# Performance work log

Measured on AMD Instinct MI355X. Metric: run time of the kernel, lower is better.

## Reference

```python
import jax, jax.numpy as jnp
import numpy as np

F_IN, F_OUT, H, L_ENC, L_DEC, HORIZON = 32, 8, 64, 2, 2, 48
B, T = 2048, 512


def _lstm_cell(x, h, c, Wih, Whh, bih, bhh):
    # PyTorch LSTMCell: gates ordered i, f, g, o
    g = x @ Wih.T + bih + h @ Whh.T + bhh
    i, f, gg, o = jnp.split(g, 4, axis=-1)
    c_new = jax.nn.sigmoid(f) * c + jax.nn.sigmoid(i) * jnp.tanh(gg)
    h_new = jax.nn.sigmoid(o) * jnp.tanh(c_new)
    return h_new, c_new


def setup_inputs() -> dict:
    key = jax.random.key(0)
    ks = jax.random.split(key, 16)
    s = 1.0 / np.sqrt(H)
    u = lambda k, shape: jax.random.uniform(k, shape, jnp.float32, -s, s)
    return {
        "X": jax.random.normal(ks[0], (B, T, F_IN), jnp.float32),
        "X_mask": jnp.ones((B, T, F_IN), jnp.float32),
        "W_emb": u(ks[1], (H, F_IN)),
        "b_emb": u(ks[2], (H,)),
        "enc_Wih": u(ks[3], (L_ENC, 4 * H, H)),
        "enc_Whh": u(ks[4], (L_ENC, 4 * H, H)),
        "enc_bih": u(ks[5], (L_ENC, 4 * H)),
        "enc_bhh": u(ks[6], (L_ENC, 4 * H)),
        "dec_Wih": u(ks[7], (L_DEC, 4 * H, H)),
        "dec_Whh": u(ks[8], (L_DEC, 4 * H, H)),
        "dec_bih": u(ks[9], (L_DEC, 4 * H)),
        "dec_bhh": u(ks[10], (L_DEC, 4 * H)),
        "W_reg": u(ks[11], (F_OUT, H)),
        "b_reg": u(ks[12], (F_OUT,)),
    }


def reference(X, X_mask, W_emb, b_emb, enc_Wih, enc_Whh, enc_bih, enc_bhh,
              dec_Wih, dec_Whh, dec_bih, dec_bhh, W_reg, b_reg):
    batch = X.shape[0]
    # Token embedding for all timesteps at once: [T, B, H]
    emb = jnp.einsum('btf,hf->tbh', X, W_emb) + b_emb

    h0 = jnp.zeros((L_ENC, batch, H), X.dtype)
    c0 = jnp.zeros((L_ENC, batch, H), X.dtype)

    def enc_step(carry, x_t):
        h, c = carry
        h_t = x_t
        hs, cs = [], []
        for i in range(L_ENC):
            h_t, c_t = _lstm_cell(h_t, h[i], c[i], enc_Wih[i], enc_Whh[i], enc_bih[i], enc_bhh[i])
            hs.append(h_t)
            cs.append(c_t)
        return (jnp.stack(hs), jnp.stack(cs)), None

    (h_enc, _), _ = jax.lax.scan(enc_step, (h0, c0), emb)

    # Decoder: hidden states initialized from encoder h, cells from zero
    c_dec0 = jnp.zeros((L_DEC, batch, H), X.dtype)

    def dec_step(carry, _):
        h, c = carry
        h_t = h[-1]
        hs, cs = [], []
        for i in range(L_DEC):
            h_t, c_t = _lstm_cell(h_t, h[i], c[i], dec_Wih[i], dec_Whh[i], dec_bih[i], dec_bhh[i])
            hs.append(h_t)
            cs.append(c_t)
        y_t = h_t @ W_reg.T + b_reg
        return (jnp.stack(hs), jnp.stack(cs)), y_t

    _, ys = jax.lax.scan(dec_step, (h_enc, c_dec0), None, length=HORIZON)
    return jnp.transpose(ys, (1, 0, 2))  # [B, horizon, F_OUT]
```

## Files before the change

kernel.cpp:

```cpp
#include <hip/hip_runtime.h>
#include <hip/hip_bf16.h>

typedef __bf16 bf16x8 __attribute__((ext_vector_type(8)));
typedef float  f32x4  __attribute__((ext_vector_type(4)));

#define MFMA16(a,b,c) __builtin_amdgcn_mfma_f32_16x16x32_bf16((a),(b),(c),0,0,0)

#if __has_builtin(__builtin_amdgcn_exp2f)
#define EXP2(x) __builtin_amdgcn_exp2f(x)
#else
#define EXP2(x) exp2f(x)
#endif
#define RCP(x) __builtin_amdgcn_rcpf(x)

#define KL  1.44269504088896340736f
#define K2L 2.88539008177792681472f

__device__ __forceinline__ bf16x8 cvt8(f32x4 a, f32x4 b){
  bf16x8 r;
  r[0]=(__bf16)a[0]; r[1]=(__bf16)a[1]; r[2]=(__bf16)a[2]; r[3]=(__bf16)a[3];
  r[4]=(__bf16)b[0]; r[5]=(__bf16)b[1]; r[6]=(__bf16)b[2]; r[7]=(__bf16)b[3];
  return r;
}
__device__ __forceinline__ f32x4 sp(float v){ return (f32x4){v,v,v,v}; }
__device__ __forceinline__ bf16x8 ld8(const float* p){
  return cvt8(*(const f32x4*)p, *(const f32x4*)(p+4));
}
__device__ __forceinline__ bf16x8 ld8s(const float* p, float s){
  f32x4 a = *(const f32x4*)p, b = *(const f32x4*)(p+4);
  return cvt8(a*sp(s), b*sp(s));
}

__device__ __forceinline__ float lstm_ew(float gi, float gf, float gg,
                                         float go, float& c){
  float Ef = EXP2(-gf);
  float Ei = EXP2(-gi);
  float gc = fminf(fmaxf(gg, -60.f), 60.f);
  float G  = EXP2(gc);
  float Rf = RCP(1.f + Ef);
  float Rig= RCP((1.f + Ei) * (1.f + G));
  c = c*Rf + (G - 1.f)*Rig;
  float Eo = EXP2(-go);
  float ch = fminf(fmaxf(c, -30.f), 30.f);
  float C2 = EXP2(ch * K2L);
  return (C2 - 1.f) * RCP((1.f + Eo) * (1.f + C2));
}

__device__ __forceinline__ float dppx8(float v){
  return __int_as_float(__builtin_amdgcn_update_dpp(
      0, __float_as_int(v), 0x128, 0xF, 0xF, true));
}
__device__ __forceinline__ float swz4(float v){
  return __int_as_float(__builtin_amdgcn_ds_swizzle(__float_as_int(v), 0x101F));
}

extern "C" __global__ void __launch_bounds__(1024, 4)
seq2seq_kernel(const float* __restrict__ X,
               const float* __restrict__ Wemb, const float* __restrict__ bemb,
               const float* __restrict__ eWih, const float* __restrict__ eWhh,
               const float* __restrict__ ebih, const float* __restrict__ ebhh,
               const float* __restrict__ dWih, const float* __restrict__ dWhh,
               const float* __restrict__ dbih, const float* __restrict__ dbhh,
               const float* __restrict__ Wreg, const float* __restrict__ breg,
               float* __restrict__ out)
{
  __shared__ __align__(16) __bf16 XA[2][8][136];
  __shared__ __align__(16) __bf16 H1s[2][8][72];

  const int tid  = (int)threadIdx.x;
  const int w    = tid >> 6;
  const int grp  = w >> 3;
  const bool g0  = (grp == 0);
  const int wt   = w & 7;
  const int lane = tid & 63;
  const int col  = lane & 15;
  const int quad = lane >> 4;
  const int row8 = col & 7;
  const int b0   = (int)blockIdx.x * 8;
  const int brow = b0 + row8;

  const bool hib = (col & 8) != 0;
  const bool qhb = (quad & 2) != 0;
  const int  ewr = 4*(quad & 1) + (hib ? 1 : 0) + (qhb ? 2 : 0);
  const int  ewu = 8*wt + (col & 7);

  for (int i = tid; i < 2*8*136; i += 1024) (&XA[0][0][0])[i]  = (__bf16)0.f;
  for (int i = tid; i < 2*8*72;  i += 1024) (&H1s[0][0][0])[i] = (__bf16)0.f;

  bf16x8 wf[8];
  float  gb[2];
#pragma unroll
  for (int ti=0; ti<2; ++ti){
    const int gate = 2*ti + (col>>3);
    const int n = 64*gate + 8*wt + (col&7);
    const float sc = (gate == 2) ? K2L : KL;
    gb[ti] = (ebih[grp*256+n] + ebhh[grp*256+n]) * sc;
#pragma unroll
    for (int ks=0; ks<4; ++ks){
      const float* srcw = (ks < 2) ? eWih : eWhh;
      wf[ti*4+ks] = ld8s(srcw + ((size_t)(grp*256+n))*64 + (ks&1)*32 + quad*8, sc);
    }
  }

  const int ue = (w&3)*16 + col;
  bf16x8 wembf;
  float eb = 0.f;
  const float* xb = X + (size_t)brow*512*32 + quad*8;
  f32x4 pa0, pb0, pa1, pb1;
  if (w < 4){
    wembf = ld8(Wemb + ue*32 + quad*8);
    eb = bemb[ue];
    pa1 = *(const f32x4*)(xb+32); pb1 = *(const f32x4*)(xb+36);
    pa0 = *(const f32x4*)(xb+64); pb0 = *(const f32x4*)(xb+68);
  }

  float cC = 0.f;

  auto EWF = [&](f32x4 A0, f32x4 A1, float& c) -> float {
    float lo0 = qhb ? A0[2] : A0[0];
    float hi0 = qhb ? A0[3] : A0[1];
    float lo1 = qhb ? A1[2] : A1[0];
    float hi1 = qhb ? A1[3] : A1[1];
    float a0s = hib ? hi0 : lo0, a0x = hib ? lo0 : hi0;
    float a1s = hib ? hi1 : lo1, a1x = hib ? lo1 : hi1;
    float r0 = dppx8(a0x), r1 = dppx8(a1x);
    float gi = hib ? r0  : a0s;
    float gf = hib ? a0s : r0;
    float gg = hib ? r1  : a1s;
    float go = hib ? a1s : r1;
    return lstm_ew(gi, gf, gg, go, c);
  };

  auto FUSED0 = [&](const int I){
    const int Px = (I+1)&1, Pr = I&1;
    bf16x8 ax0 = *(const bf16x8*)&XA[Px][row8][ 0 + quad*8];
    bf16x8 ax1 = *(const bf16x8*)&XA[Px][row8][32 + quad*8];
    bf16x8 ah0 = *(const bf16x8*)&XA[Pr][row8][64 + quad*8];
    bf16x8 ah1 = *(const bf16x8*)&XA[Pr][row8][96 + quad*8];
    f32x4 A0 = sp(gb[0]), A1 = sp(gb[1]);
    A0=MFMA16(ax0,wf[0],A0); A1=MFMA16(ax0,wf[4],A1);
    A0=MFMA16(ax1,wf[1],A0); A1=MFMA16(ax1,wf[5],A1);
    A0=MFMA16(ah0,wf[2],A0); A1=MFMA16(ah0,wf[6],A1);
    A0=MFMA16(ah1,wf[3],A0); A1=MFMA16(ah1,wf[7],A1);
    if (I < 510 && w < 4){
      const int s = I&1;
      f32x4 xr0 = s ? pa1 : pa0, xr1 = s ? pb1 : pb0;
      f32x4 ea = MFMA16(cvt8(xr0,xr1), wembf, sp(eb));
      int tn = I+4; if (tn > 511) tn = 511;
      f32x4 na = *(const f32x4*)(xb + (size_t)tn*32);
      f32x4 nb = *(const f32x4*)(xb + (size_t)tn*32 + 4);
      if (s){ pa1=na; pb1=nb; } else { pa0=na; pb0=nb; }
      if (quad < 2){
#pragma unroll
        for (int r=0; r<4; ++r) XA[s][quad*4+r][ue] = (__bf16)ea[r];
      }
    }
    XA[Px][ewr][64+ewu] = (__bf16)EWF(A0, A1, cC);
  };

  auto FUSED1 = [&](const int I){
    const int Px = (I+1)&1, Pr = I&1;
    bf16x8 ah0 = *(const bf16x8*)&XA[Pr][row8][64 + quad*8];
    bf16x8 ah1 = *(const bf16x8*)&XA[Pr][row8][96 + quad*8];
    bf16x8 ag0 = *(const bf16x8*)&H1s[Px][row8][quad*8];
    bf16x8 ag1 = *(const bf16x8*)&H1s[Px][row8][32 + quad*8];
    f32x4 A0 = sp(gb[0]), A1 = sp(gb[1]);
    A0=MFMA16(ah0,wf[0],A0); A1=MFMA16(ah0,wf[4],A1);
    A0=MFMA16(ah1,wf[1],A0); A1=MFMA16(ah1,wf[5],A1);
    A0=MFMA16(ag0,wf[2],A0); A1=MFMA16(ag0,wf[6],A1);
    A0=MFMA16(ag1,wf[3],A0); A1=MFMA16(ag1,wf[7],A1);
    H1s[Pr][ewr][ewu] = (__bf16)EWF(A0, A1, cC);
  };

  __syncthreads();

  if (w < 4){
    f32x4 x0a = *(const f32x4*)xb, x0b = *(const f32x4*)(xb+4);
    f32x4 e0 = MFMA16(cvt8(x0a,x0b), wembf, sp(eb));
    if (quad < 2){
#pragma unroll
      for (int r=0; r<4; ++r) XA[0][quad*4+r][ue] = (__bf16)e0[r];
    }
  }
  __syncthreads();
  if (g0) FUSED0(-1);
  __syncthreads();

#define SLOT(I) { if (g0) FUSED0(I); else FUSED1(I); __syncthreads(); }
  for (int ii=0; ii<255; ++ii){
    SLOT(2*ii)
    SLOT(2*ii+1)
  }
  SLOT(510)
#undef SLOT

  if (!g0) FUSED1(511);
  __syncthreads();

  for (int idx = tid; idx < 8*64; idx += 1024){
    XA[1][idx>>6][idx&63] = H1s[1][idx>>6][idx&63];
  }
  bf16x8 wr0 = ld8(Wreg + (col&7)*64 +  0 + quad*8);
  bf16x8 wr1 = ld8(Wreg + (col&7)*64 + 32 + quad*8);
  const float rb = breg[col&7];
  const int  gated = col >> 2;
  const float scd = (gated == 2) ? K2L : KL;
  float gbd[2];
#pragma unroll
  for (int l=0; l<2; ++l){
    const int n = 64*gated + 4*w + (col&3);
    gbd[l] = (dbih[l*256+n] + dbhh[l*256+n]) * scd;
#pragma unroll
    for (int ks=0; ks<4; ++ks){
      const float* srcw = (ks < 2) ? dWih : dWhh;
      wf[l*4+ks] = ld8s(srcw + ((size_t)(l*256+n))*64 + (ks&1)*32 + quad*8, scd);
    }
  }
  const bool b0d = (gated & 1) != 0;
  const bool b1d = (gated & 2) != 0;
  const int  rd  = 4*(quad & 1) + (b1d ? 1 : 0) + (qhb ? 2 : 0);
  const int  udj = 4*w + (col & 3);
  float cD0 = 0.f, cD1 = 0.f;
  __syncthreads();

  auto EWD = [&](f32x4 B, float& c) -> float {
    float lo  = qhb ? B[2] : B[0];
    float hi2 = qhb ? B[3] : B[1];
    float a  = b1d ? hi2 : lo;
    float ax = b1d ? lo  : hi2;
    float pA = swz4(a);
    float pB = swz4(ax);
    float qA = dppx8(ax);
    float qB = dppx8(pB);
    float gi = b1d ? (b0d?qB:qA) : (b0d?pA:a);
    float gf = b1d ? (b0d?qA:qB) : (b0d?a:pA);
    float gg = b1d ? (b0d?pA:a) : (b0d?qB:qA);
    float go = b1d ? (b0d?a:pA) : (b0d?qA:qB);
    return lstm_ew(gi, gf, gg, go, c);
  };

  auto Ystore = [&](const int t){
    const int hp = t&1;
    f32x4 ya = sp(rb);
    bf16x8 y0 = *(const bf16x8*)&H1s[hp][row8][quad*8];
    bf16x8 y1 = *(const bf16x8*)&H1s[hp][row8][32 + quad*8];
    ya = MFMA16(y0, wr0, ya);
    ya = MFMA16(y1, wr1, ya);
    if (quad < 2 && col < 8){
#pragma unroll
      for (int r=0; r<4; ++r)
        out[((size_t)(b0 + quad*4 + r)*48 + t)*8 + col] = ya[r];
    }
  };

#define DSTEP(T) {                                                         \
    const int P = (T)&1, Pm = P^1;                                         \
    {                                                                      \
      bf16x8 ax0 = *(const bf16x8*)&XA[Pm][row8][ 0 + quad*8];             \
      bf16x8 ax1 = *(const bf16x8*)&XA[Pm][row8][32 + quad*8];             \
      bf16x8 ah0 = *(const bf16x8*)&XA[Pm][row8][64 + quad*8];             \
      bf16x8 ah1 = *(const bf16x8*)&XA[Pm][row8][96 + quad*8];             \
      f32x4 B0 = sp(gbd[0]);                                               \
      B0=MFMA16(ax0,wf[0],B0); B0=MFMA16(ax1,wf[1],B0);                    \
      B0=MFMA16(ah0,wf[2],B0); B0=MFMA16(ah1,wf[3],B0);                    \
      float h = EWD(B0, cD0);                                              \
      if (!b0d) XA[P][rd][64+udj] = (__bf16)h;                             \
      if ((T) && w == 0) Ystore((T)-1);                                    \
    }                                                                      \
    __syncthreads();                                                       \
    {                                                                      \
      bf16x8 ah0 = *(const bf16x8*)&XA[P][row8][64 + quad*8];              \
      bf16x8 ah1 = *(const bf16x8*)&XA[P][row8][96 + quad*8];              \
      bf16x8 ag0 = *(const bf16x8*)&H1s[Pm][row8][ 0 + quad*8];            \
      bf16x8 ag1 = *(const bf16x8*)&H1s[Pm][row8][32 + quad*8];            \
      f32x4 B1 = sp(gbd[1]);                                               \
      B1=MFMA16(ah0,wf[4],B1); B1=MFMA16(ah1,wf[5],B1);                    \
      B1=MFMA16(ag0,wf[6],B1); B1=MFMA16(ag1,wf[7],B1);                    \
      float h = EWD(B1, cD1);                                              \
      if (!b0d){ H1s[P][rd][udj] = (__bf16)h; XA[P][rd][udj] = (__bf16)h; }\
    }                                                                      \
    __syncthreads();                                                       \
  }

  for (int tt=0; tt<24; ++tt){
    DSTEP(2*tt)
    DSTEP(2*tt+1)
  }
#undef DSTEP
  if (w == 0) Ystore(47);
}

extern "C" void kernel_launch(void* const* d_in, const int* in_sizes, int n_in,
                              void* d_out, int out_size, void* d_ws, size_t ws_size,
                              hipStream_t stream)
{
  (void)in_sizes; (void)n_in; (void)out_size; (void)d_ws; (void)ws_size;
  const float* X    = (const float*)d_in[0];
  const float* Wemb = (const float*)d_in[2];
  const float* bemb = (const float*)d_in[3];
  const float* eWih = (const float*)d_in[4];
  const float* eWhh = (const float*)d_in[5];
  const float* ebih = (const float*)d_in[6];
  const float* ebhh = (const float*)d_in[7];
  const float* dWih = (const float*)d_in[8];
  const float* dWhh = (const float*)d_in[9];
  const float* dbih = (const float*)d_in[10];
  const float* dbhh = (const float*)d_in[11];
  const float* Wreg = (const float*)d_in[12];
  const float* breg = (const float*)d_in[13];
  float* out = (float*)d_out;

  seq2seq_kernel<<<dim3(256), dim3(1024), 0, stream>>>(
      X, Wemb, bemb, eWih, eWhh, ebih, ebhh,
      dWih, dWhh, dbih, dbhh, Wreg, breg, out);
}
```

Before: 602.9 us.

## Halve batch rows per block and give each wave all four gates

Each block now handles 4 batch rows with 512 threads (8 waves) across 512 blocks, instead of 8 rows with 1024 threads across 256 blocks. Each wave computes all four gate tiles for its 16 hidden units, so the DPP/swizzle shuffles that gathered gates across lanes go away, and the decoder now splits its two layers across wave groups rather than running both in every wave. This trades cross-lane exchange and barrier cost against more MFMA work wasted on padded rows (only 4 of 16 used) and more weight registers per wave.

```diff
diff --git a/kernel.cpp b/kernel.cpp
--- a/kernel.cpp
+++ b/kernel.cpp
@@ -46,15 +46,7 @@
   return (C2 - 1.f) * RCP((1.f + Eo) * (1.f + C2));
 }
 
-__device__ __forceinline__ float dppx8(float v){
-  return __int_as_float(__builtin_amdgcn_update_dpp(
-      0, __float_as_int(v), 0x128, 0xF, 0xF, true));
-}
-__device__ __forceinline__ float swz4(float v){
-  return __int_as_float(__builtin_amdgcn_ds_swizzle(__float_as_int(v), 0x101F));
-}
-
-extern "C" __global__ void __launch_bounds__(1024, 4)
+extern "C" __global__ void __launch_bounds__(512, 4)
 seq2seq_kernel(const float* __restrict__ X,
                const float* __restrict__ Wemb, const float* __restrict__ bemb,
                const float* __restrict__ eWih, const float* __restrict__ eWhh,
@@ -64,122 +56,117 @@
                const float* __restrict__ Wreg, const float* __restrict__ breg,
                float* __restrict__ out)
 {
-  __shared__ __align__(16) __bf16 XA[2][8][136];
-  __shared__ __align__(16) __bf16 H1s[2][8][72];
+  __shared__ __align__(16) __bf16 XA[2][4][144];
+  __shared__ __align__(16) __bf16 H1s[2][4][80];
 
   const int tid  = (int)threadIdx.x;
   const int w    = tid >> 6;
-  const int grp  = w >> 3;
-  const bool g0  = (grp == 0);
-  const int wt   = w & 7;
+  const bool g0  = (w < 4);
+  const int wt   = w & 3;
   const int lane = tid & 63;
   const int col  = lane & 15;
   const int quad = lane >> 4;
-  const int row8 = col & 7;
-  const int b0   = (int)blockIdx.x * 8;
-  const int brow = b0 + row8;
-
-  const bool hib = (col & 8) != 0;
-  const bool qhb = (quad & 2) != 0;
-  const int  ewr = 4*(quad & 1) + (hib ? 1 : 0) + (qhb ? 2 : 0);
-  const int  ewu = 8*wt + (col & 7);
-
-  for (int i = tid; i < 2*8*136; i += 1024) (&XA[0][0][0])[i]  = (__bf16)0.f;
-  for (int i = tid; i < 2*8*72;  i += 1024) (&H1s[0][0][0])[i] = (__bf16)0.f;
-
-  bf16x8 wf[8];
-  float  gb[2];
-#pragma unroll
-  for (int ti=0; ti<2; ++ti){
-    const int gate = 2*ti + (col>>3);
-    const int n = 64*gate + 8*wt + (col&7);
-    const float sc = (gate == 2) ? K2L : KL;
-    gb[ti] = (ebih[grp*256+n] + ebhh[grp*256+n]) * sc;
+  const int r4   = col & 3;
+  const int b0   = (int)blockIdx.x * 4;
+  const int ucol = 16*wt + col;
+  const bool qb1 = (quad & 1) != 0;
+  const bool qb2 = (quad & 2) != 0;
+
+  for (int i = tid; i < 2*4*144; i += 512) (&XA[0][0][0])[i]  = (__bf16)0.f;
+  for (int i = tid; i < 2*4*80;  i += 512) (&H1s[0][0][0])[i] = (__bf16)0.f;
+
+  bf16x8 wf[16];
+  float  gb[4];
+#pragma unroll
+  for (int ti=0; ti<4; ++ti){
+    const int n = (g0 ? 0 : 256) + 64*ti + ucol;
+    const float sc = (ti == 2) ? K2L : KL;
+    gb[ti] = (ebih[n] + ebhh[n]) * sc;
 #pragma unroll
     for (int ks=0; ks<4; ++ks){
       const float* srcw = (ks < 2) ? eWih : eWhh;
-      wf[ti*4+ks] = ld8s(srcw + ((size_t)(grp*256+n))*64 + (ks&1)*32 + quad*8, sc);
-    }
-  }
-
-  const int ue = (w&3)*16 + col;
+      wf[ti*4+ks] = ld8s(srcw + (size_t)n*64 + (ks&1)*32 + quad*8, sc);
+    }
+  }
+
   bf16x8 wembf;
   float eb = 0.f;
-  const float* xb = X + (size_t)brow*512*32 + quad*8;
-  f32x4 pa0, pb0, pa1, pb1;
-  if (w < 4){
-    wembf = ld8(Wemb + ue*32 + quad*8);
-    eb = bemb[ue];
-    pa1 = *(const f32x4*)(xb+32); pb1 = *(const f32x4*)(xb+36);
-    pa0 = *(const f32x4*)(xb+64); pb0 = *(const f32x4*)(xb+68);
+  const float* xb = X + (size_t)(b0 + r4)*512*32 + quad*8;
+  f32x4 pa, pb;
+  if (g0){
+    wembf = ld8(Wemb + ucol*32 + quad*8);
+    eb = bemb[ucol];
+    pa = *(const f32x4*)(xb+32); pb = *(const f32x4*)(xb+36);
   }
 
   float cC = 0.f;
 
-  auto EWF = [&](f32x4 A0, f32x4 A1, float& c) -> float {
-    float lo0 = qhb ? A0[2] : A0[0];
-    float hi0 = qhb ? A0[3] : A0[1];
-    float lo1 = qhb ? A1[2] : A1[0];
-    float hi1 = qhb ? A1[3] : A1[1];
-    float a0s = hib ? hi0 : lo0, a0x = hib ? lo0 : hi0;
-    float a1s = hib ? hi1 : lo1, a1x = hib ? lo1 : hi1;
-    float r0 = dppx8(a0x), r1 = dppx8(a1x);
-    float gi = hib ? r0  : a0s;
-    float gf = hib ? a0s : r0;
-    float gg = hib ? r1  : a1s;
-    float go = hib ? a1s : r1;
-    return lstm_ew(gi, gf, gg, go, c);
+  auto pick = [&](f32x4 v) -> float {
+    float s0 = qb2 ? v[2] : v[0];
+    float s1 = qb2 ? v[3] : v[1];
+    return qb1 ? s1 : s0;
   };
 
   auto FUSED0 = [&](const int I){
     const int Px = (I+1)&1, Pr = I&1;
-    bf16x8 ax0 = *(const bf16x8*)&XA[Px][row8][ 0 + quad*8];
-    bf16x8 ax1 = *(const bf16x8*)&XA[Px][row8][32 + quad*8];
-    bf16x8 ah0 = *(const bf16x8*)&XA[Pr][row8][64 + quad*8];
-    bf16x8 ah1 = *(const bf16x8*)&XA[Pr][row8][96 + quad*8];
-    f32x4 A0 = sp(gb[0]), A1 = sp(gb[1]);
-    A0=MFMA16(ax0,wf[0],A0); A1=MFMA16(ax0,wf[4],A1);
-    A0=MFMA16(ax1,wf[1],A0); A1=MFMA16(ax1,wf[5],A1);
-    A0=MFMA16(ah0,wf[2],A0); A1=MFMA16(ah0,wf[6],A1);
-    A0=MFMA16(ah1,wf[3],A0); A1=MFMA16(ah1,wf[7],A1);
-    if (I < 510 && w < 4){
-      const int s = I&1;
-      f32x4 xr0 = s ? pa1 : pa0, xr1 = s ? pb1 : pb0;
-      f32x4 ea = MFMA16(cvt8(xr0,xr1), wembf, sp(eb));
-      int tn = I+4; if (tn > 511) tn = 511;
-      f32x4 na = *(const f32x4*)(xb + (size_t)tn*32);
-      f32x4 nb = *(const f32x4*)(xb + (size_t)tn*32 + 4);
-      if (s){ pa1=na; pb1=nb; } else { pa0=na; pb0=nb; }
-      if (quad < 2){
-#pragma unroll
-        for (int r=0; r<4; ++r) XA[s][quad*4+r][ue] = (__bf16)ea[r];
+    bf16x8 axe;
+    if (I < 510){
+      axe = cvt8(pa, pb);
+      int tn = I+3; if (tn > 511) tn = 511;
+      pa = *(const f32x4*)(xb + (size_t)tn*32);
+      pb = *(const f32x4*)(xb + (size_t)tn*32 + 4);
+    }
+    bf16x8 ax0 = *(const bf16x8*)&XA[Px][r4][ 0 + quad*8];
+    bf16x8 ax1 = *(const bf16x8*)&XA[Px][r4][32 + quad*8];
+    bf16x8 ah0 = *(const bf16x8*)&XA[Pr][r4][64 + quad*8];
+    bf16x8 ah1 = *(const bf16x8*)&XA[Pr][r4][96 + quad*8];
+    f32x4 A0 = sp(gb[0]), A1 = sp(gb[1]), A2 = sp(gb[2]), A3 = sp(gb[3]);
+    A0=MFMA16(ax0,wf[ 0],A0); A1=MFMA16(ax0,wf[ 4],A1);
+    A2=MFMA16(ax0,wf[ 8],A2); A3=MFMA16(ax0,wf[12],A3);
+    A0=MFMA16(ax1,wf[ 1],A0); A1=MFMA16(ax1,wf[ 5],A1);
+    A2=MFMA16(ax1,wf[ 9],A2); A3=MFMA16(ax1,wf[13],A3);
+    A0=MFMA16(ah0,wf[ 2],A0); A1=MFMA16(ah0,wf[ 6],A1);
+    A2=MFMA16(ah0,wf[10],A2); A3=MFMA16(ah0,wf[14],A3);
+    A0=MFMA16(ah1,wf[ 3],A0); A1=MFMA16(ah1,wf[ 7],A1);
+    A2=MFMA16(ah1,wf[11],A2); A3=MFMA16(ah1,wf[15],A3);
+    if (I < 510){
+      f32x4 ea = MFMA16(axe, wembf, sp(eb));
+      if (quad == 0){
+#pragma unroll
+        for (int r=0; r<4; ++r) XA[I&1][r][ucol] = (__bf16)ea[r];
       }
     }
-    XA[Px][ewr][64+ewu] = (__bf16)EWF(A0, A1, cC);
+    XA[Px][quad][64+ucol] =
+        (__bf16)lstm_ew(pick(A0), pick(A1), pick(A2), pick(A3), cC);
   };
 
   auto FUSED1 = [&](const int I){
     const int Px = (I+1)&1, Pr = I&1;
-    bf16x8 ah0 = *(const bf16x8*)&XA[Pr][row8][64 + quad*8];
-    bf16x8 ah1 = *(const bf16x8*)&XA[Pr][row8][96 + quad*8];
-    bf16x8 ag0 = *(const bf16x8*)&H1s[Px][row8][quad*8];
-    bf16x8 ag1 = *(const bf16x8*)&H1s[Px][row8][32 + quad*8];
-    f32x4 A0 = sp(gb[0]), A1 = sp(gb[1]);
-    A0=MFMA16(ah0,wf[0],A0); A1=MFMA16(ah0,wf[4],A1);
-    A0=MFMA16(ah1,wf[1],A0); A1=MFMA16(ah1,wf[5],A1);
-    A0=MFMA16(ag0,wf[2],A0); A1=MFMA16(ag0,wf[6],A1);
-    A0=MFMA16(ag1,wf[3],A0); A1=MFMA16(ag1,wf[7],A1);
-    H1s[Pr][ewr][ewu] = (__bf16)EWF(A0, A1, cC);
-  };
-
-  __syncthreads();
-
-  if (w < 4){
+    bf16x8 ah0 = *(const bf16x8*)&XA[Pr][r4][64 + quad*8];
+    bf16x8 ah1 = *(const bf16x8*)&XA[Pr][r4][96 + quad*8];
+    bf16x8 ag0 = *(const bf16x8*)&H1s[Px][r4][     quad*8];
+    bf16x8 ag1 = *(const bf16x8*)&H1s[Px][r4][32 + quad*8];
+    f32x4 A0 = sp(gb[0]), A1 = sp(gb[1]), A2 = sp(gb[2]), A3 = sp(gb[3]);
+    A0=MFMA16(ah0,wf[ 0],A0); A1=MFMA16(ah0,wf[ 4],A1);
+    A2=MFMA16(ah0,wf[ 8],A2); A3=MFMA16(ah0,wf[12],A3);
+    A0=MFMA16(ah1,wf[ 1],A0); A1=MFMA16(ah1,wf[ 5],A1);
+    A2=MFMA16(ah1,wf[ 9],A2); A3=MFMA16(ah1,wf[13],A3);
+    A0=MFMA16(ag0,wf[ 2],A0); A1=MFMA16(ag0,wf[ 6],A1);
+    A2=MFMA16(ag0,wf[10],A2); A3=MFMA16(ag0,wf[14],A3);
+    A0=MFMA16(ag1,wf[ 3],A0); A1=MFMA16(ag1,wf[ 7],A1);
+    A2=MFMA16(ag1,wf[11],A2); A3=MFMA16(ag1,wf[15],A3);
+    H1s[Pr][quad][ucol] =
+        (__bf16)lstm_ew(pick(A0), pick(A1), pick(A2), pick(A3), cC);
+  };
+
+  __syncthreads();
+
+  if (g0){
     f32x4 x0a = *(const f32x4*)xb, x0b = *(const f32x4*)(xb+4);
     f32x4 e0 = MFMA16(cvt8(x0a,x0b), wembf, sp(eb));
-    if (quad < 2){
-#pragma unroll
-      for (int r=0; r<4; ++r) XA[0][quad*4+r][ue] = (__bf16)e0[r];
+    if (quad == 0){
+#pragma unroll
+      for (int r=0; r<4; ++r) XA[0][r][ucol] = (__bf16)e0[r];
     }
   }
   __syncthreads();
@@ -197,97 +184,84 @@
   if (!g0) FUSED1(511);
   __syncthreads();
 
-  for (int idx = tid; idx < 8*64; idx += 1024){
+  for (int idx = tid; idx < 4*64; idx += 512)
     XA[1][idx>>6][idx&63] = H1s[1][idx>>6][idx&63];
-  }
-  bf16x8 wr0 = ld8(Wreg + (col&7)*64 +  0 + quad*8);
+
+  float gbd[4];
+#pragma unroll
+  for (int ti=0; ti<4; ++ti){
+    const int n = (g0 ? 0 : 256) + 64*ti + ucol;
+    const float sc = (ti == 2) ? K2L : KL;
+    gbd[ti] = (dbih[n] + dbhh[n]) * sc;
+#pragma unroll
+    for (int ks=0; ks<4; ++ks){
+      const float* srcw = (ks < 2) ? dWih : dWhh;
+      wf[ti*4+ks] = ld8s(srcw + (size_t)n*64 + (ks&1)*32 + quad*8, sc);
+    }
+  }
+  bf16x8 wr0 = ld8(Wreg + (col&7)*64 +      quad*8);
   bf16x8 wr1 = ld8(Wreg + (col&7)*64 + 32 + quad*8);
   const float rb = breg[col&7];
-  const int  gated = col >> 2;
-  const float scd = (gated == 2) ? K2L : KL;
-  float gbd[2];
-#pragma unroll
-  for (int l=0; l<2; ++l){
-    const int n = 64*gated + 4*w + (col&3);
-    gbd[l] = (dbih[l*256+n] + dbhh[l*256+n]) * scd;
-#pragma unroll
-    for (int ks=0; ks<4; ++ks){
-      const float* srcw = (ks < 2) ? dWih : dWhh;
-      wf[l*4+ks] = ld8s(srcw + ((size_t)(l*256+n))*64 + (ks&1)*32 + quad*8, scd);
-    }
-  }
-  const bool b0d = (gated & 1) != 0;
-  const bool b1d = (gated & 2) != 0;
-  const int  rd  = 4*(quad & 1) + (b1d ? 1 : 0) + (qhb ? 2 : 0);
-  const int  udj = 4*w + (col & 3);
-  float cD0 = 0.f, cD1 = 0.f;
-  __syncthreads();
-
-  auto EWD = [&](f32x4 B, float& c) -> float {
-    float lo  = qhb ? B[2] : B[0];
-    float hi2 = qhb ? B[3] : B[1];
-    float a  = b1d ? hi2 : lo;
-    float ax = b1d ? lo  : hi2;
-    float pA = swz4(a);
-    float pB = swz4(ax);
-    float qA = dppx8(ax);
-    float qB = dppx8(pB);
-    float gi = b1d ? (b0d?qB:qA) : (b0d?pA:a);
-    float gf = b1d ? (b0d?qA:qB) : (b0d?a:pA);
-    float gg = b1d ? (b0d?pA:a) : (b0d?qB:qA);
-    float go = b1d ? (b0d?a:pA) : (b0d?qA:qB);
-    return lstm_ew(gi, gf, gg, go, c);
-  };
+  float cD = 0.f;
+  __syncthreads();
 
   auto Ystore = [&](const int t){
     const int hp = t&1;
     f32x4 ya = sp(rb);
-    bf16x8 y0 = *(const bf16x8*)&H1s[hp][row8][quad*8];
-    bf16x8 y1 = *(const bf16x8*)&H1s[hp][row8][32 + quad*8];
+    bf16x8 y0 = *(const bf16x8*)&H1s[hp][r4][     quad*8];
+    bf16x8 y1 = *(const bf16x8*)&H1s[hp][r4][32 + quad*8];
     ya = MFMA16(y0, wr0, ya);
     ya = MFMA16(y1, wr1, ya);
-    if (quad < 2 && col < 8){
+    if (quad == 0 && col < 8){
 #pragma unroll
       for (int r=0; r<4; ++r)
-        out[((size_t)(b0 + quad*4 + r)*48 + t)*8 + col] = ya[r];
-    }
-  };
-
-#define DSTEP(T) {                                                         \
-    const int P = (T)&1, Pm = P^1;                                         \
-    {                                                                      \
-      bf16x8 ax0 = *(const bf16x8*)&XA[Pm][row8][ 0 + quad*8];             \
-      bf16x8 ax1 = *(const bf16x8*)&XA[Pm][row8][32 + quad*8];             \
-      bf16x8 ah0 = *(const bf16x8*)&XA[Pm][row8][64 + quad*8];             \
-      bf16x8 ah1 = *(const bf16x8*)&XA[Pm][row8][96 + quad*8];             \
-      f32x4 B0 = sp(gbd[0]);                                               \
-      B0=MFMA16(ax0,wf[0],B0); B0=MFMA16(ax1,wf[1],B0);                    \
-      B0=MFMA16(ah0,wf[2],B0); B0=MFMA16(ah1,wf[3],B0);                    \
-      float h = EWD(B0, cD0);                                              \
-      if (!b0d) XA[P][rd][64+udj] = (__bf16)h;                             \
-      if ((T) && w == 0) Ystore((T)-1);                                    \
-    }                                                                      \
-    __syncthreads();                                                       \
-    {                                                                      \
-      bf16x8 ah0 = *(const bf16x8*)&XA[P][row8][64 + quad*8];              \
-      bf16x8 ah1 = *(const bf16x8*)&XA[P][row8][96 + quad*8];              \
-      bf16x8 ag0 = *(const bf16x8*)&H1s[Pm][row8][ 0 + quad*8];            \
-      bf16x8 ag1 = *(const bf16x8*)&H1s[Pm][row8][32 + quad*8];            \
-      f32x4 B1 = sp(gbd[1]);                                               \
-      B1=MFMA16(ah0,wf[4],B1); B1=MFMA16(ah1,wf[5],B1);                    \
-      B1=MFMA16(ag0,wf[6],B1); B1=MFMA16(ag1,wf[7],B1);                    \
-      float h = EWD(B1, cD1);                                              \
-      if (!b0d){ H1s[P][rd][udj] = (__bf16)h; XA[P][rd][udj] = (__bf16)h; }\
-    }                                                                      \
-    __syncthreads();                                                       \
-  }
-
-  for (int tt=0; tt<24; ++tt){
-    DSTEP(2*tt)
-    DSTEP(2*tt+1)
-  }
-#undef DSTEP
-  if (w == 0) Ystore(47);
+        out[((size_t)(b0 + r)*48 + t)*8 + col] = ya[r];
+    }
+  };
+
+  for (int t=0; t<48; ++t){
+    const int P = t&1, Pm = P^1;
+    if (g0){
+      bf16x8 ax0 = *(const bf16x8*)&XA[Pm][r4][ 0 + quad*8];
+      bf16x8 ax1 = *(const bf16x8*)&XA[Pm][r4][32 + quad*8];
+      bf16x8 ah0 = *(const bf16x8*)&XA[Pm][r4][64 + quad*8];
+      bf16x8 ah1 = *(const bf16x8*)&XA[Pm][r4][96 + quad*8];
+      f32x4 A0 = sp(gbd[0]), A1 = sp(gbd[1]), A2 = sp(gbd[2]), A3 = sp(gbd[3]);
+      A0=MFMA16(ax0,wf[ 0],A0); A1=MFMA16(ax0,wf[ 4],A1);
+      A2=MFMA16(ax0,wf[ 8],A2); A3=MFMA16(ax0,wf[12],A3);
+      A0=MFMA16(ax1,wf[ 1],A0); A1=MFMA16(ax1,wf[ 5],A1);
+      A2=MFMA16(ax1,wf[ 9],A2); A3=MFMA16(ax1,wf[13],A3);
+      A0=MFMA16(ah0,wf[ 2],A0); A1=MFMA16(ah0,wf[ 6],A1);
+      A2=MFMA16(ah0,wf[10],A2); A3=MFMA16(ah0,wf[14],A3);
+      A0=MFMA16(ah1,wf[ 3],A0); A1=MFMA16(ah1,wf[ 7],A1);
+      A2=MFMA16(ah1,wf[11],A2); A3=MFMA16(ah1,wf[15],A3);
+      XA[P][quad][64+ucol] =
+          (__bf16)lstm_ew(pick(A0), pick(A1), pick(A2), pick(A3), cD);
+    } else if (w == 4 && t) {
+      Ystore(t-1);
+    }
+    __syncthreads();
+    if (!g0){
+      bf16x8 ah0 = *(const bf16x8*)&XA[P][r4][64 + quad*8];
+      bf16x8 ah1 = *(const bf16x8*)&XA[P][r4][96 + quad*8];
+      bf16x8 ag0 = *(const bf16x8*)&H1s[Pm][r4][     quad*8];
+      bf16x8 ag1 = *(const bf16x8*)&H1s[Pm][r4][32 + quad*8];
+      f32x4 A0 = sp(gbd[0]), A1 = sp(gbd[1]), A2 = sp(gbd[2]), A3 = sp(gbd[3]);
+      A0=MFMA16(ah0,wf[ 0],A0); A1=MFMA16(ah0,wf[ 4],A1);
+      A2=MFMA16(ah0,wf[ 8],A2); A3=MFMA16(ah0,wf[12],A3);
+      A0=MFMA16(ah1,wf[ 1],A0); A1=MFMA16(ah1,wf[ 5],A1);
+      A2=MFMA16(ah1,wf[ 9],A2); A3=MFMA16(ah1,wf[13],A3);
+      A0=MFMA16(ag0,wf[ 2],A0); A1=MFMA16(ag0,wf[ 6],A1);
+      A2=MFMA16(ag0,wf[10],A2); A3=MFMA16(ag0,wf[14],A3);
+      A0=MFMA16(ag1,wf[ 3],A0); A1=MFMA16(ag1,wf[ 7],A1);
+      A2=MFMA16(ag1,wf[11],A2); A3=MFMA16(ag1,wf[15],A3);
+      float h = lstm_ew(pick(A0), pick(A1), pick(A2), pick(A3), cD);
+      H1s[P][quad][ucol] = (__bf16)h;
+      XA[P][quad][ucol]  = (__bf16)h;
+    }
+    __syncthreads();
+  }
+  if (w == 4) Ystore(47);
 }
 
 extern "C" void kernel_launch(void* const* d_in, const int* in_sizes, int n_in,
@@ -310,7 +284,7 @@
   const float* breg = (const float*)d_in[13];
   float* out = (float*)d_out;
 
-  seq2seq_kernel<<<dim3(256), dim3(1024), 0, stream>>>(
+  seq2seq_kernel<<<dim3(512), dim3(512), 0, stream>>>(
       X, Wemb, bemb, eWih, eWhh, ebih, ebhh,
       dWih, dWhh, dbih, dbhh, Wreg, breg, out);
 }
```

Result: slower. 1.092 ms (+81.1%).
